# Performance work log

Hardware: AMD Instinct MI355X
Metric: run time of the kernel (lower is better)

The kernel has to match this reference:

```python
import jax, jax.numpy as jnp
import numpy as np


def _sdpa(q, k, v):
    # scaled dot-product attention, no dropout (eval mode)
    d = q.shape[-1]
    s = jnp.einsum('bhqd,bhkd->bhqk', q, k) / jnp.sqrt(jnp.asarray(d, q.dtype))
    a = jax.nn.softmax(s, axis=-1)
    return jnp.einsum('bhqk,bhkd->bhqd', a, v)


def setup_inputs() -> dict:
    key = jax.random.key(0)
    ks = jax.random.split(key, 9)
    BC, H, N, d = 128, 4, 1024, 64
    B, C = 4, 32
    C_ch, l, r, TC = 32, 16, 8, 144
    half_dim = H * d  # 256
    q_t = jax.random.normal(ks[0], (BC, H, N, d), jnp.float32)
    k_t = jax.random.normal(ks[1], (BC, H, N, d), jnp.float32)
    v_t = jax.random.normal(ks[2], (BC, H, N, d), jnp.float32)
    L_n = jax.random.normal(ks[3], (B * N, C_ch, C_ch), jnp.float32)
    slots = jax.random.normal(ks[4], (1, l, half_dim), jnp.float32) * 0.02
    pack_q_w = jax.random.normal(ks[5], (half_dim, half_dim), jnp.float32) * 0.02
    mu_proto_factors = jax.random.normal(ks[6], (l, TC, r), jnp.float32) * 0.02
    spd_beta = jnp.array([0.5], jnp.float32)
    channel_idx = jax.random.randint(ks[7], (C_ch,), 0, TC)
    return dict(q_t=q_t, k_t=k_t, v_t=v_t, L_n=L_n, slots=slots,
                pack_q_w=pack_q_w, mu_proto_factors=mu_proto_factors,
                spd_beta=spd_beta, channel_idx=channel_idx, C=C)


def _spd_distances(L_per_sample, mu_proto_factors, channel_idx):
    # L_per_sample: (B, N, C_ch, C_ch) -> distances (B, l, N)
    B, N, C_ch, _ = L_per_sample.shape
    l = mu_proto_factors.shape[0]
    U_sub = mu_proto_factors[:, channel_idx]            # (l, C_ch, r)
    L_flat = L_per_sample.reshape(B, N, C_ch * C_ch)    # (B, N, C_ch^2)
    L_sqnorm = jnp.sum(L_flat * L_flat, axis=-1)        # (B, N)
    UtU = jnp.einsum('lcr,lcs->lrs', U_sub, U_sub)      # (l, r, r)
    mu_sqnorm = jnp.sum(UtU * UtU, axis=(-2, -1))       # (l,)
    mu_sub = jnp.einsum('lcr,ldr->lcd', U_sub, U_sub)   # (l, C_ch, C_ch)
    mu_flat = mu_sub.reshape(l, C_ch * C_ch)
    cross = jnp.einsum('bni,li->bnl', L_flat, mu_flat)  # (B, N, l)
    dist_sq = L_sqnorm[..., None] + mu_sqnorm[None, None, :] - 2.0 * cross
    dist_sq = jnp.clip(dist_sq, 0.0, None)
    return jnp.sqrt(dist_sq).transpose(0, 2, 1)         # (B, l, N)


def reference(q_t, k_t, v_t, L_n, slots, pack_q_w, mu_proto_factors,
              spd_beta, channel_idx, C):
    BC, H, N, d = q_t.shape
    l = slots.shape[1]
    scale = d ** (-0.5)
    # pack queries: Linear(bias=False) then split heads; slots are shared across batch
    pq = slots[0] @ pack_q_w.T                          # (l, H*d)
    pq = pq.reshape(l, H, d).transpose(1, 0, 2)         # (H, l, d)
    pack_score = jnp.einsum('hld,bhnd->bhln', pq, k_t) * scale  # (BC, H, l, N)
    # SPD geometric bias (L_n is detached in the original)
    B = BC // C
    C_ch = L_n.shape[1]
    L_per_sample = jax.lax.stop_gradient(L_n).reshape(B, N, C_ch, C_ch)
    spd_dist_b = _spd_distances(L_per_sample, mu_proto_factors, channel_idx)  # (B, l, N)
    spd_dist = jnp.repeat(spd_dist_b, C, axis=0)        # (BC, l, N)
    pack_score = pack_score - spd_beta[0] * spd_dist[:, None, :, :]
    pack_attn = jax.nn.softmax(pack_score, axis=-1)
    packed = jnp.einsum('bhln,bhnd->bhld', pack_attn, v_t)  # (BC, H, l, d)
    processed = _sdpa(packed, packed, packed)               # (BC, H, l, d)
    out = _sdpa(q_t, processed, processed)                  # (BC, H, N, d)
    return out
```

## Files before the change

kernel.cpp:

```cpp
#include <hip/hip_runtime.h>
#include <hip/hip_bf16.h>

typedef unsigned short ushort_t;

__device__ __forceinline__ float bf2f(ushort_t u) {
    return __uint_as_float(((unsigned int)u) << 16);
}
__device__ __forceinline__ ushort_t f2bf(float f) {
    __hip_bfloat16 h = __float2bfloat16(f);
    return *reinterpret_cast<ushort_t*>(&h);
}

__global__ void k_pq(const float* __restrict__ slots,
                     const float* __restrict__ W,
                     float* __restrict__ pq) {
    __shared__ float SL[4096];
    int j = threadIdx.x;
#pragma unroll
    for (int i = 0; i < 16; ++i) SL[j + i * 256] = slots[j + i * 256];
    __syncthreads();
    float acc[16];
#pragma unroll
    for (int l = 0; l < 16; ++l) acc[l] = 0.f;
    const float4* wr = (const float4*)(W + j * 256);
    for (int g = 0; g < 64; ++g) {
        float4 wv = wr[g];
#pragma unroll
        for (int l = 0; l < 16; ++l) {
            const float* sl = &SL[l * 256 + g * 4];
            acc[l] += wv.x * sl[0] + wv.y * sl[1] + wv.z * sl[2] + wv.w * sl[3];
        }
    }
    int h = j >> 6, d = j & 63;
#pragma unroll
    for (int l = 0; l < 16; ++l) pq[(h * 16 + l) * 64 + d] = acc[l];
}

__global__ void k_mu(const float* __restrict__ mu,
                     const int* __restrict__ cidx,
                     float* __restrict__ mu_flat,
                     float* __restrict__ mu_sq) {
    int l = blockIdx.x;
    __shared__ float U[256];
    __shared__ float utu[64];
    int t = threadIdx.x;
    {
        int c = t >> 3, r = t & 7;
        U[t] = mu[(l * 144 + cidx[c]) * 8 + r];
    }
    __syncthreads();
#pragma unroll
    for (int i = 0; i < 4; ++i) {
        int e = t + i * 256;
        int c = e >> 5, dd = e & 31;
        float acc = 0.f;
#pragma unroll
        for (int r = 0; r < 8; ++r) acc += U[c * 8 + r] * U[dd * 8 + r];
        mu_flat[l * 1024 + e] = acc;
    }
    if (t < 64) {
        int r = t >> 3, s = t & 7;
        float acc = 0.f;
        for (int c = 0; c < 32; ++c) acc += U[c * 8 + r] * U[c * 8 + s];
        utu[t] = acc;
    }
    __syncthreads();
    if (t == 0) {
        float acc = 0.f;
        for (int i = 0; i < 64; ++i) acc += utu[i] * utu[i];
        mu_sq[l] = acc;
    }
}

__global__ __launch_bounds__(256) void k_dist(const float* __restrict__ Ln,
                                              const float* __restrict__ mu_flat,
                                              const float* __restrict__ mu_sq,
                                              float* __restrict__ dist) {
    int blk = blockIdx.x;
    int chunk = blk & 3;
    int lg = (blk >> 2) & 3;
    int bs = blk >> 4;
    __shared__ float MF[4][1024];
    int t = threadIdx.x;
#pragma unroll
    for (int i = 0; i < 16; ++i) {
        int e = t + i * 256;
        MF[e >> 10][e & 1023] = mu_flat[(lg * 4 + (e >> 10)) * 1024 + (e & 1023)];
    }
    __syncthreads();
    int n = chunk * 256 + t;
    const float4* lr = (const float4*)(Ln + ((size_t)(bs * 1024 + n)) * 1024);
    float lsq = 0.f;
    float cr[4] = {0.f, 0.f, 0.f, 0.f};
    for (int g = 0; g < 256; ++g) {
        float4 lv = lr[g];
        lsq += lv.x * lv.x + lv.y * lv.y + lv.z * lv.z + lv.w * lv.w;
#pragma unroll
        for (int ll = 0; ll < 4; ++ll) {
            const float* mf = &MF[ll][g * 4];
            cr[ll] += lv.x * mf[0] + lv.y * mf[1] + lv.z * mf[2] + lv.w * mf[3];
        }
    }
#pragma unroll
    for (int ll = 0; ll < 4; ++ll) {
        int l = lg * 4 + ll;
        float d2 = lsq + mu_sq[l] - 2.f * cr[ll];
        dist[(bs * 16 + l) * 1024 + n] = sqrtf(fmaxf(d2, 0.f));
    }
}

__global__ __launch_bounds__(1024) void k_pack2(const float* __restrict__ kt,
                                                const float* __restrict__ vt,
                                                const float* __restrict__ pq,
                                                const float* __restrict__ dist,
                                                const float* __restrict__ beta_p,
                                                float* __restrict__ packed) {
    int bc = blockIdx.x >> 2, h = blockIdx.x & 3;
    int bs = bc >> 5;
    __shared__ __align__(16) float PQ[1024];
    __shared__ __align__(16) ushort_t PB[16 * 1024];
    __shared__ __align__(16) float VST[64 * 64];
    __shared__ float wred[16 * 16];
    __shared__ float gred[16];
    int t = threadIdx.x;
    int lane = t & 63, w = t >> 6;
    PQ[t] = pq[h * 1024 + t];
    float beta = beta_p[0];
    __syncthreads();

    const size_t base = ((size_t)blockIdx.x) * 65536;
    const float4* kr = (const float4*)(kt + base + (size_t)t * 64);
    float sc[16];
#pragma unroll
    for (int l = 0; l < 16; ++l) sc[l] = 0.f;
    for (int g = 0; g < 16; ++g) {
        float4 kv = kr[g];
#pragma unroll
        for (int l = 0; l < 16; ++l) {
            const float* pql = &PQ[l * 64 + g * 4];
            sc[l] += kv.x * pql[0] + kv.y * pql[1] + kv.z * pql[2] + kv.w * pql[3];
        }
    }
#pragma unroll
    for (int l = 0; l < 16; ++l)
        sc[l] = 0.125f * sc[l] - beta * dist[(bs * 16 + l) * 1024 + t];

#pragma unroll
    for (int l = 0; l < 16; ++l) {
        float m = sc[l];
#pragma unroll
        for (int off = 32; off >= 1; off >>= 1) m = fmaxf(m, __shfl_xor(m, off));
        if (lane == 0) wred[l * 16 + w] = m;
    }
    __syncthreads();
    if (t < 16) {
        float m = -1e30f;
#pragma unroll
        for (int w2 = 0; w2 < 16; ++w2) m = fmaxf(m, wred[t * 16 + w2]);
        gred[t] = m;
    }
    __syncthreads();

    float ex[16];
#pragma unroll
    for (int l = 0; l < 16; ++l) {
        ex[l] = __expf(sc[l] - gred[l]);
        float s = ex[l];
#pragma unroll
        for (int off = 32; off >= 1; off >>= 1) s += __shfl_xor(s, off);
        if (lane == 0) wred[l * 16 + w] = s;
    }
    __syncthreads();
    if (t < 16) {
        float s = 0.f;
#pragma unroll
        for (int w2 = 0; w2 < 16; ++w2) s += wred[t * 16 + w2];
        gred[t] = 1.f / s;
    }
    __syncthreads();
#pragma unroll
    for (int l = 0; l < 16; ++l) PB[l * 1024 + t] = f2bf(ex[l] * gred[l]);
    __syncthreads();

    const float4* vr = (const float4*)(vt + base);
    int l = w, d = lane;
    float acc = 0.f;
    for (int ch = 0; ch < 16; ++ch) {
        __syncthreads();
        ((float4*)VST)[t] = vr[ch * 1024 + t];
        __syncthreads();
        const ushort_t* pb = &PB[l * 1024 + ch * 64];
#pragma unroll 4
        for (int j = 0; j < 64; ++j) acc += bf2f(pb[j]) * VST[j * 64 + d];
    }
    packed[((size_t)blockIdx.x) * 1024 + t] = acc;
}

__global__ void k_proc(const float* __restrict__ packed, float* __restrict__ proc) {
    int bh = blockIdx.x;
    __shared__ float P[1024];
    __shared__ float A[256];
    int t = threadIdx.x;
#pragma unroll
    for (int i = 0; i < 4; ++i) P[t + i * 256] = packed[(size_t)bh * 1024 + t + i * 256];
    __syncthreads();
    {
        int i = t >> 4, j = t & 15;
        float acc = 0.f;
#pragma unroll
        for (int dd = 0; dd < 64; ++dd) acc += P[i * 64 + dd] * P[j * 64 + dd];
        A[t] = acc * 0.125f;
    }
    __syncthreads();
    if (t < 16) {
        float m = -1e30f;
#pragma unroll
        for (int j = 0; j < 16; ++j) m = fmaxf(m, A[t * 16 + j]);
        float s = 0.f;
#pragma unroll
        for (int j = 0; j < 16; ++j) { float e = __expf(A[t * 16 + j] - m); A[t * 16 + j] = e; s += e; }
        float inv = 1.f / s;
#pragma unroll
        for (int j = 0; j < 16; ++j) A[t * 16 + j] *= inv;
    }
    __syncthreads();
#pragma unroll
    for (int i = 0; i < 4; ++i) {
        int e = t + i * 256;
        int r = e >> 6, d = e & 63;
        float acc = 0.f;
#pragma unroll
        for (int j = 0; j < 16; ++j) acc += A[r * 16 + j] * P[j * 64 + d];
        proc[(size_t)bh * 1024 + e] = acc;
    }
}

__global__ __launch_bounds__(256) void k_final(const float* __restrict__ qt,
                                               const float* __restrict__ proc,
                                               float* __restrict__ out) {
    int bh = blockIdx.x >> 2, ch = blockIdx.x & 3;
    __shared__ float P[1024];
    int t = threadIdx.x;
#pragma unroll
    for (int i = 0; i < 4; ++i) P[t + i * 256] = proc[(size_t)bh * 1024 + t + i * 256];
    __syncthreads();
    int n = ch * 256 + t;
    const float4* qr = (const float4*)(qt + ((size_t)bh * 1024 + n) * 64);
    float qf[64];
#pragma unroll
    for (int g = 0; g < 16; ++g) {
        float4 qv = qr[g];
        qf[g * 4 + 0] = qv.x; qf[g * 4 + 1] = qv.y;
        qf[g * 4 + 2] = qv.z; qf[g * 4 + 3] = qv.w;
    }
    float sj[16];
    float m = -1e30f;
#pragma unroll
    for (int j = 0; j < 16; ++j) {
        float acc = 0.f;
#pragma unroll
        for (int dd = 0; dd < 64; ++dd) acc += qf[dd] * P[j * 64 + dd];
        sj[j] = acc * 0.125f;
        m = fmaxf(m, sj[j]);
    }
    float s = 0.f;
#pragma unroll
    for (int j = 0; j < 16; ++j) { sj[j] = __expf(sj[j] - m); s += sj[j]; }
    float inv = 1.f / s;
#pragma unroll
    for (int j = 0; j < 16; ++j) sj[j] *= inv;
    float4* orow = (float4*)(out + ((size_t)bh * 1024 + n) * 64);
#pragma unroll
    for (int g = 0; g < 16; ++g) {
        float4 pk;
        float* pp = (float*)&pk;
#pragma unroll
        for (int kk = 0; kk < 4; ++kk) {
            int d = g * 4 + kk;
            float acc = 0.f;
#pragma unroll
            for (int j = 0; j < 16; ++j) acc += sj[j] * P[j * 64 + d];
            pp[kk] = acc;
        }
        orow[g] = pk;
    }
}

extern "C" void kernel_launch(void* const* d_in, const int* in_sizes, int n_in,
                              void* d_out, int out_size, void* d_ws, size_t ws_size,
                              hipStream_t stream) {
    const float* q     = (const float*)d_in[0];
    const float* k     = (const float*)d_in[1];
    const float* v     = (const float*)d_in[2];
    const float* Ln    = (const float*)d_in[3];
    const float* slots = (const float*)d_in[4];
    const float* W     = (const float*)d_in[5];
    const float* mu    = (const float*)d_in[6];
    const float* beta  = (const float*)d_in[7];
    const int* cidx    = (const int*)d_in[8];

    float* ws     = (float*)d_ws;
    float* pq     = ws;
    float* muf    = ws + 4096;
    float* musq   = ws + 20480;
    float* dist   = ws + 20496;
    float* packed = ws + 86032;
    float* proc   = ws + 610320;

    k_pq   <<<1,    256, 0, stream>>>(slots, W, pq);
    k_mu   <<<16,   256, 0, stream>>>(mu, cidx, muf, musq);
    k_dist <<<64,   256, 0, stream>>>(Ln, muf, musq, dist);
    k_pack2<<<512, 1024, 0, stream>>>(k, v, pq, dist, beta, packed);
    k_proc <<<512,  256, 0, stream>>>(packed, proc);
    k_final<<<2048, 256, 0, stream>>>(q, proc, (float*)d_out);
}
```

Measured before the change: 640.1 us.

## Re-parallelize pq, dist, pack and final kernels for coalescing and occupancy

k_pq is spread over 16 blocks, one per slot. k_dist now gives each row of L to 16 lanes, which read it coalesced and combine partial sums with shuffles, over 256 blocks. k_pack2's PV product is reorganized into float4 per-lane accumulators over split j-ranges, with a prefetch of the next V chunk and a padded probability buffer to reduce LDS conflicts. k_final has each group of 4 lanes handle a quarter of d for two rows, giving coalesced float4 q loads and out stores. Together these aim to raise memory coalescing and parallelism on the bandwidth-heavy stages, at the cost of more shuffles and registers.

```diff
diff --git a/kernel.cpp b/kernel.cpp
--- a/kernel.cpp
+++ b/kernel.cpp
@@ -11,29 +11,23 @@
     return *reinterpret_cast<ushort_t*>(&h);
 }
 
-__global__ void k_pq(const float* __restrict__ slots,
-                     const float* __restrict__ W,
-                     float* __restrict__ pq) {
-    __shared__ float SL[4096];
-    int j = threadIdx.x;
-#pragma unroll
-    for (int i = 0; i < 16; ++i) SL[j + i * 256] = slots[j + i * 256];
-    __syncthreads();
-    float acc[16];
-#pragma unroll
-    for (int l = 0; l < 16; ++l) acc[l] = 0.f;
+__global__ __launch_bounds__(256) void k_pq(const float* __restrict__ slots,
+                                            const float* __restrict__ W,
+                                            float* __restrict__ pq) {
+    int l = blockIdx.x, j = threadIdx.x;
+    __shared__ float SL[256];
+    SL[j] = slots[l * 256 + j];
+    __syncthreads();
     const float4* wr = (const float4*)(W + j * 256);
+    float acc = 0.f;
+#pragma unroll 8
     for (int g = 0; g < 64; ++g) {
         float4 wv = wr[g];
-#pragma unroll
-        for (int l = 0; l < 16; ++l) {
-            const float* sl = &SL[l * 256 + g * 4];
-            acc[l] += wv.x * sl[0] + wv.y * sl[1] + wv.z * sl[2] + wv.w * sl[3];
-        }
+        const float* sl = &SL[g * 4];
+        acc += wv.x * sl[0] + wv.y * sl[1] + wv.z * sl[2] + wv.w * sl[3];
     }
     int h = j >> 6, d = j & 63;
-#pragma unroll
-    for (int l = 0; l < 16; ++l) pq[(h * 16 + l) * 64 + d] = acc[l];
+    pq[(h * 16 + l) * 64 + d] = acc;
 }
 
 __global__ void k_mu(const float* __restrict__ mu,
@@ -77,36 +71,37 @@
                                               const float* __restrict__ mu_sq,
                                               float* __restrict__ dist) {
     int blk = blockIdx.x;
-    int chunk = blk & 3;
-    int lg = (blk >> 2) & 3;
-    int bs = blk >> 4;
-    __shared__ float MF[4][1024];
-    int t = threadIdx.x;
-#pragma unroll
-    for (int i = 0; i < 16; ++i) {
-        int e = t + i * 256;
-        MF[e >> 10][e & 1023] = mu_flat[(lg * 4 + (e >> 10)) * 1024 + (e & 1023)];
-    }
-    __syncthreads();
-    int n = chunk * 256 + t;
+    int nchunk = blk & 63, bs = blk >> 6;
+    int t = threadIdx.x;
+    int ln = t & 15, rid = t >> 4;
+    int n = nchunk * 16 + rid;
     const float4* lr = (const float4*)(Ln + ((size_t)(bs * 1024 + n)) * 1024);
+    const float4* mf = (const float4*)mu_flat;
     float lsq = 0.f;
-    float cr[4] = {0.f, 0.f, 0.f, 0.f};
-    for (int g = 0; g < 256; ++g) {
-        float4 lv = lr[g];
+    float cr[16];
+#pragma unroll
+    for (int l = 0; l < 16; ++l) cr[l] = 0.f;
+#pragma unroll 2
+    for (int g = 0; g < 16; ++g) {
+        float4 lv = lr[g * 16 + ln];
         lsq += lv.x * lv.x + lv.y * lv.y + lv.z * lv.z + lv.w * lv.w;
 #pragma unroll
-        for (int ll = 0; ll < 4; ++ll) {
-            const float* mf = &MF[ll][g * 4];
-            cr[ll] += lv.x * mf[0] + lv.y * mf[1] + lv.z * mf[2] + lv.w * mf[3];
+        for (int l = 0; l < 16; ++l) {
+            float4 mv = mf[l * 256 + g * 16 + ln];
+            cr[l] += lv.x * mv.x + lv.y * mv.y + lv.z * mv.z + lv.w * mv.w;
         }
     }
 #pragma unroll
-    for (int ll = 0; ll < 4; ++ll) {
-        int l = lg * 4 + ll;
-        float d2 = lsq + mu_sq[l] - 2.f * cr[ll];
-        dist[(bs * 16 + l) * 1024 + n] = sqrtf(fmaxf(d2, 0.f));
-    }
+    for (int off = 8; off >= 1; off >>= 1) {
+        lsq += __shfl_xor(lsq, off);
+#pragma unroll
+        for (int l = 0; l < 16; ++l) cr[l] += __shfl_xor(cr[l], off);
+    }
+    float mycr = cr[0];
+#pragma unroll
+    for (int l = 1; l < 16; ++l) if (ln == l) mycr = cr[l];
+    float d2 = lsq + mu_sq[ln] - 2.f * mycr;
+    dist[((size_t)(bs * 16 + ln)) * 1024 + n] = sqrtf(fmaxf(d2, 0.f));
 }
 
 __global__ __launch_bounds__(1024) void k_pack2(const float* __restrict__ kt,
@@ -118,8 +113,8 @@
     int bc = blockIdx.x >> 2, h = blockIdx.x & 3;
     int bs = bc >> 5;
     __shared__ __align__(16) float PQ[1024];
-    __shared__ __align__(16) ushort_t PB[16 * 1024];
-    __shared__ __align__(16) float VST[64 * 64];
+    __shared__ __align__(16) ushort_t PB[16 * 1032];
+    __shared__ __align__(16) float VST[4096];
     __shared__ float wred[16 * 16];
     __shared__ float gred[16];
     int t = threadIdx.x;
@@ -143,7 +138,7 @@
     }
 #pragma unroll
     for (int l = 0; l < 16; ++l)
-        sc[l] = 0.125f * sc[l] - beta * dist[(bs * 16 + l) * 1024 + t];
+        sc[l] = 0.125f * sc[l] - beta * dist[((size_t)(bs * 16 + l)) * 1024 + t];
 
 #pragma unroll
     for (int l = 0; l < 16; ++l) {
@@ -179,21 +174,44 @@
     }
     __syncthreads();
 #pragma unroll
-    for (int l = 0; l < 16; ++l) PB[l * 1024 + t] = f2bf(ex[l] * gred[l]);
-    __syncthreads();
+    for (int l = 0; l < 16; ++l) PB[l * 1032 + t] = f2bf(ex[l] * gred[l]);
 
     const float4* vr = (const float4*)(vt + base);
-    int l = w, d = lane;
-    float acc = 0.f;
+    int jg = w >> 2;
+    int sl = (w & 3) * 4 + (lane >> 4);
+    int dg = lane & 15;
+    float4 acc; acc.x = acc.y = acc.z = acc.w = 0.f;
+    float4* VST4 = (float4*)VST;
+    float4 pre = vr[t];
     for (int ch = 0; ch < 16; ++ch) {
         __syncthreads();
-        ((float4*)VST)[t] = vr[ch * 1024 + t];
+        VST4[t] = pre;
         __syncthreads();
-        const ushort_t* pb = &PB[l * 1024 + ch * 64];
-#pragma unroll 4
-        for (int j = 0; j < 64; ++j) acc += bf2f(pb[j]) * VST[j * 64 + d];
-    }
-    packed[((size_t)blockIdx.x) * 1024 + t] = acc;
+        if (ch < 15) pre = vr[(ch + 1) * 1024 + t];
+        const ushort_t* pbp = &PB[sl * 1032 + ch * 64 + jg * 16];
+        uint4 pw0 = *(const uint4*)(pbp);
+        uint4 pw1 = *(const uint4*)(pbp + 8);
+        const float4* vb = VST4 + jg * 256 + dg;
+        unsigned wbuf[8] = {pw0.x, pw0.y, pw0.z, pw0.w, pw1.x, pw1.y, pw1.z, pw1.w};
+#pragma unroll
+        for (int pr = 0; pr < 8; ++pr) {
+            float p0 = __uint_as_float(wbuf[pr] << 16);
+            float p1 = __uint_as_float(wbuf[pr] & 0xffff0000u);
+            float4 v0 = vb[(2 * pr) * 16];
+            float4 v1 = vb[(2 * pr + 1) * 16];
+            acc.x += p0 * v0.x + p1 * v1.x;
+            acc.y += p0 * v0.y + p1 * v1.y;
+            acc.z += p0 * v0.z + p1 * v1.z;
+            acc.w += p0 * v0.w + p1 * v1.w;
+        }
+    }
+    __syncthreads();
+    VST4[jg * 256 + sl * 16 + dg] = acc;
+    __syncthreads();
+    int l = t >> 6, d = t & 63;
+    float sum = VST[l * 64 + d] + VST[1024 + l * 64 + d]
+              + VST[2048 + l * 64 + d] + VST[3072 + l * 64 + d];
+    packed[((size_t)blockIdx.x) * 1024 + t] = sum;
 }
 
 __global__ void k_proc(const float* __restrict__ packed, float* __restrict__ proc) {
@@ -238,52 +256,70 @@
 __global__ __launch_bounds__(256) void k_final(const float* __restrict__ qt,
                                                const float* __restrict__ proc,
                                                float* __restrict__ out) {
-    int bh = blockIdx.x >> 2, ch = blockIdx.x & 3;
-    __shared__ float P[1024];
-    int t = threadIdx.x;
-#pragma unroll
-    for (int i = 0; i < 4; ++i) P[t + i * 256] = proc[(size_t)bh * 1024 + t + i * 256];
-    __syncthreads();
-    int n = ch * 256 + t;
-    const float4* qr = (const float4*)(qt + ((size_t)bh * 1024 + n) * 64);
-    float qf[64];
-#pragma unroll
-    for (int g = 0; g < 16; ++g) {
-        float4 qv = qr[g];
-        qf[g * 4 + 0] = qv.x; qf[g * 4 + 1] = qv.y;
-        qf[g * 4 + 2] = qv.z; qf[g * 4 + 3] = qv.w;
-    }
-    float sj[16];
-    float m = -1e30f;
+    int bh = blockIdx.x >> 3, chunk = blockIdx.x & 7;
+    __shared__ __align__(16) float P[1024];
+    int t = threadIdx.x;
+    ((float4*)P)[t] = ((const float4*)(proc + (size_t)bh * 1024))[t];
+    __syncthreads();
+    int q = t & 3, rid = t >> 2;
+    int n0 = chunk * 128 + rid, n1 = n0 + 64;
+    const float4* q0 = (const float4*)(qt + ((size_t)bh * 1024 + n0) * 64) + q * 4;
+    const float4* q1 = (const float4*)(qt + ((size_t)bh * 1024 + n1) * 64) + q * 4;
+    float4 qa0 = q0[0], qa1 = q0[1], qa2 = q0[2], qa3 = q0[3];
+    float4 qb0 = q1[0], qb1 = q1[1], qb2 = q1[2], qb3 = q1[3];
+    const float4* P4 = (const float4*)P + q * 4;
+
+    float s0[16], s1[16];
 #pragma unroll
     for (int j = 0; j < 16; ++j) {
-        float acc = 0.f;
-#pragma unroll
-        for (int dd = 0; dd < 64; ++dd) acc += qf[dd] * P[j * 64 + dd];
-        sj[j] = acc * 0.125f;
-        m = fmaxf(m, sj[j]);
-    }
-    float s = 0.f;
-#pragma unroll
-    for (int j = 0; j < 16; ++j) { sj[j] = __expf(sj[j] - m); s += sj[j]; }
-    float inv = 1.f / s;
-#pragma unroll
-    for (int j = 0; j < 16; ++j) sj[j] *= inv;
-    float4* orow = (float4*)(out + ((size_t)bh * 1024 + n) * 64);
-#pragma unroll
-    for (int g = 0; g < 16; ++g) {
-        float4 pk;
-        float* pp = (float*)&pk;
-#pragma unroll
-        for (int kk = 0; kk < 4; ++kk) {
-            int d = g * 4 + kk;
-            float acc = 0.f;
-#pragma unroll
-            for (int j = 0; j < 16; ++j) acc += sj[j] * P[j * 64 + d];
-            pp[kk] = acc;
-        }
-        orow[g] = pk;
-    }
+        float4 p0 = P4[j * 16 + 0], p1 = P4[j * 16 + 1];
+        float4 p2 = P4[j * 16 + 2], p3 = P4[j * 16 + 3];
+        float a = qa0.x * p0.x + qa0.y * p0.y + qa0.z * p0.z + qa0.w * p0.w
+                + qa1.x * p1.x + qa1.y * p1.y + qa1.z * p1.z + qa1.w * p1.w
+                + qa2.x * p2.x + qa2.y * p2.y + qa2.z * p2.z + qa2.w * p2.w
+                + qa3.x * p3.x + qa3.y * p3.y + qa3.z * p3.z + qa3.w * p3.w;
+        float b = qb0.x * p0.x + qb0.y * p0.y + qb0.z * p0.z + qb0.w * p0.w
+                + qb1.x * p1.x + qb1.y * p1.y + qb1.z * p1.z + qb1.w * p1.w
+                + qb2.x * p2.x + qb2.y * p2.y + qb2.z * p2.z + qb2.w * p2.w
+                + qb3.x * p3.x + qb3.y * p3.y + qb3.z * p3.z + qb3.w * p3.w;
+        a += __shfl_xor(a, 1); a += __shfl_xor(a, 2);
+        b += __shfl_xor(b, 1); b += __shfl_xor(b, 2);
+        s0[j] = a * 0.125f; s1[j] = b * 0.125f;
+    }
+    float m0 = s0[0], m1 = s1[0];
+#pragma unroll
+    for (int j = 1; j < 16; ++j) { m0 = fmaxf(m0, s0[j]); m1 = fmaxf(m1, s1[j]); }
+    float t0 = 0.f, t1 = 0.f;
+#pragma unroll
+    for (int j = 0; j < 16; ++j) {
+        s0[j] = __expf(s0[j] - m0); t0 += s0[j];
+        s1[j] = __expf(s1[j] - m1); t1 += s1[j];
+    }
+    float i0 = 1.f / t0, i1 = 1.f / t1;
+#pragma unroll
+    for (int j = 0; j < 16; ++j) { s0[j] *= i0; s1[j] *= i1; }
+
+    float4 o00, o01, o02, o03, o10, o11, o12, o13;
+    o00.x=o00.y=o00.z=o00.w=0.f; o01=o00; o02=o00; o03=o00;
+    o10=o00; o11=o00; o12=o00; o13=o00;
+#pragma unroll
+    for (int j = 0; j < 16; ++j) {
+        float4 p0 = P4[j * 16 + 0], p1 = P4[j * 16 + 1];
+        float4 p2 = P4[j * 16 + 2], p3 = P4[j * 16 + 3];
+        float a = s0[j], b = s1[j];
+        o00.x += a * p0.x; o00.y += a * p0.y; o00.z += a * p0.z; o00.w += a * p0.w;
+        o01.x += a * p1.x; o01.y += a * p1.y; o01.z += a * p1.z; o01.w += a * p1.w;
+        o02.x += a * p2.x; o02.y += a * p2.y; o02.z += a * p2.z; o02.w += a * p2.w;
+        o03.x += a * p3.x; o03.y += a * p3.y; o03.z += a * p3.z; o03.w += a * p3.w;
+        o10.x += b * p0.x; o10.y += b * p0.y; o10.z += b * p0.z; o10.w += b * p0.w;
+        o11.x += b * p1.x; o11.y += b * p1.y; o11.z += b * p1.z; o11.w += b * p1.w;
+        o12.x += b * p2.x; o12.y += b * p2.y; o12.z += b * p2.z; o12.w += b * p2.w;
+        o13.x += b * p3.x; o13.y += b * p3.y; o13.z += b * p3.z; o13.w += b * p3.w;
+    }
+    float4* w0 = (float4*)(out + ((size_t)bh * 1024 + n0) * 64) + q * 4;
+    float4* w1 = (float4*)(out + ((size_t)bh * 1024 + n1) * 64) + q * 4;
+    w0[0] = o00; w0[1] = o01; w0[2] = o02; w0[3] = o03;
+    w1[0] = o10; w1[1] = o11; w1[2] = o12; w1[3] = o13;
 }
 
 extern "C" void kernel_launch(void* const* d_in, const int* in_sizes, int n_in,
@@ -307,10 +343,10 @@
     float* packed = ws + 86032;
     float* proc   = ws + 610320;
 
-    k_pq   <<<1,    256, 0, stream>>>(slots, W, pq);
+    k_pq   <<<16,   256, 0, stream>>>(slots, W, pq);
     k_mu   <<<16,   256, 0, stream>>>(mu, cidx, muf, musq);
-    k_dist <<<64,   256, 0, stream>>>(Ln, muf, musq, dist);
+    k_dist <<<256,  256, 0, stream>>>(Ln, muf, musq, dist);
     k_pack2<<<512, 1024, 0, stream>>>(k, v, pq, dist, beta, packed);
     k_proc <<<512,  256, 0, stream>>>(packed, proc);
-    k_final<<<2048, 256, 0, stream>>>(q, proc, (float*)d_out);
-}
+    k_final<<<4096, 256, 0, stream>>>(q, proc, (float*)d_out);
+}
```

Result: faster. 600.3 us (-6.2%).
